# Kernel tuning notes

Measured on AMD Instinct MI355X. Metric: run time of the kernel, lower is better.

The kernel has to match this reference:

```python
import jax, jax.numpy as jnp
import numpy as np

B, S, C = 2, 2048, 512
E, H = 512, 8
HD = E // H
SCALE = HD ** -0.5


def setup_inputs() -> dict:
    key = jax.random.key(0)
    ks = jax.random.split(key, 10)
    s = 1.0 / np.sqrt(C)
    return {
        "x": jax.random.normal(ks[0], (B, S, C), dtype=jnp.float32),
        "dist_map": jax.random.uniform(ks[1], (B, H, S, S), dtype=jnp.float32),
        "mask": jax.random.randint(ks[2], (B, S), 0, 2, dtype=jnp.int32),
        "Wq": jax.random.normal(ks[3], (E, C), dtype=jnp.float32) * s,
        "bq": jnp.zeros((E,), dtype=jnp.float32),
        "Wk": jax.random.normal(ks[4], (E, C), dtype=jnp.float32) * s,
        "bk": jnp.zeros((E,), dtype=jnp.float32),
        "Wv": jax.random.normal(ks[5], (E, C), dtype=jnp.float32) * s,
        "bv": jnp.zeros((E,), dtype=jnp.float32),
        "Wo": jax.random.normal(ks[6], (E, E), dtype=jnp.float32) * (1.0 / np.sqrt(E)),
        "bo": jnp.zeros((E,), dtype=jnp.float32),
    }


def reference(x, dist_map, mask, Wq, bq, Wk, bk, Wv, bv, Wo, bo):
    # NOTE: faithful to original torch code: .view(B, H, S, HD) without transpose
    q = (x @ Wq.T + bq).reshape(B, H, S, HD)
    k = (x @ Wk.T + bk).reshape(B, H, S, HD)
    v = (x @ Wv.T + bv).reshape(B, H, S, HD)
    attn = jnp.einsum('bhqd,bhkd->bhqk', q, k)
    pad = mask.astype(bool)[:, None, None, :]  # [B,1,1,S]
    attn = jnp.where(pad, jnp.float32(-10000.0), attn)
    attn = jax.nn.softmax(attn * SCALE, axis=-1)
    attn = (attn + dist_map) * 0.5  # post-softmax dist_map blend
    # dropout p=0.0 -> identity
    attn_probs = attn
    ctx = jnp.einsum('bhal,bhlv->bhav', attn_probs, v)  # [B,H,S,HD]
    ctx = ctx.transpose(0, 2, 1, 3).reshape(B, S, E)
    out = ctx @ Wo.T + bo
    return (out, attn_probs)
```

## Files before the change

### kernel.cpp

```cpp
#include <hip/hip_runtime.h>
#include <stdint.h>

typedef __attribute__((ext_vector_type(4))) float  f32x4;
typedef __attribute__((ext_vector_type(8))) short  short8;
typedef __attribute__((ext_vector_type(4))) short  short4v;

#define MFMA16(a,b,c) __builtin_amdgcn_mfma_f32_16x16x32_bf16((a),(b),(c),0,0,0)

static __device__ __forceinline__ unsigned short f2bf(float f) {
    unsigned int u = __float_as_uint(f);
    u += 0x7FFFu + ((u >> 16) & 1u);
    return (unsigned short)(u >> 16);
}
static __device__ __forceinline__ float bflo(unsigned int v) { return __uint_as_float(v << 16); }
static __device__ __forceinline__ float bfhi(unsigned int v) { return __uint_as_float(v & 0xFFFF0000u); }
static __device__ __forceinline__ float bf2f(unsigned short v) { return __uint_as_float(((unsigned int)v) << 16); }
static __device__ __forceinline__ unsigned int packbf(float a, float b) {
    return (unsigned int)f2bf(a) | ((unsigned int)f2bf(b) << 16);
}


__global__ __launch_bounds__(256) void qkv_gemm(
    const float* __restrict__ x,
    const float* __restrict__ Wq, const float* __restrict__ bq,
    const float* __restrict__ Wk, const float* __restrict__ bk,
    const float* __restrict__ Wv, const float* __restrict__ bv,
    unsigned short* __restrict__ Qb, unsigned short* __restrict__ Kb,
    unsigned short* __restrict__ Vb)
{
    __shared__ unsigned short As[128 * 40];
    __shared__ unsigned short Bs[128 * 40];

    const int tid  = threadIdx.x;
    const int lane = tid & 63;
    const int wid  = tid >> 6;
    const int g = lane >> 4, c = lane & 15;
    const int wr = wid >> 1, wc = wid & 1;
    const int bm    = blockIdx.x;
    const int widx  = blockIdx.y >> 2;
    const int ntile = blockIdx.y & 3;

    const float* W    = (widx == 0) ? Wq : (widx == 1) ? Wk : Wv;
    const float* bias = (widx == 0) ? bq : (widx == 1) ? bk : bv;
    unsigned short* Y = (widx == 0) ? Qb : (widx == 1) ? Kb : Vb;
    const float* Abase = x + (size_t)bm * 128 * 512;
    const float* Bbase = W + (size_t)ntile * 128 * 512;

    f32x4 acc[4][4];
    #pragma unroll
    for (int m = 0; m < 4; m++)
        #pragma unroll
        for (int n = 0; n < 4; n++) acc[m][n] = (f32x4){0.f, 0.f, 0.f, 0.f};

    for (int kk = 0; kk < 512; kk += 32) {
        #pragma unroll
        for (int i = 0; i < 4; i++) {
            int f  = i * 256 + tid;
            int rr = f >> 3;
            int cc = (f & 7) * 4;
            f32x4 va = *(const f32x4*)(Abase + rr * 512 + kk + cc);
            f32x4 vb = *(const f32x4*)(Bbase + rr * 512 + kk + cc);
            short4v sa, sb;
            #pragma unroll
            for (int q = 0; q < 4; q++) { sa[q] = (short)f2bf(va[q]); sb[q] = (short)f2bf(vb[q]); }
            *(short4v*)(&As[rr * 40 + cc]) = sa;
            *(short4v*)(&Bs[rr * 40 + cc]) = sb;
        }
        __syncthreads();

        short8 af[4], bfr[4];
        #pragma unroll
        for (int m = 0; m < 4; m++) af[m]  = *(const short8*)(&As[(wr * 64 + m * 16 + c) * 40 + g * 8]);
        #pragma unroll
        for (int n = 0; n < 4; n++) bfr[n] = *(const short8*)(&Bs[(wc * 64 + n * 16 + c) * 40 + g * 8]);
        #pragma unroll
        for (int m = 0; m < 4; m++)
            #pragma unroll
            for (int n = 0; n < 4; n++)
                acc[m][n] = MFMA16(af[m], bfr[n], acc[m][n]);
        __syncthreads();
    }

    #pragma unroll
    for (int n = 0; n < 4; n++) {
        int colW = ntile * 128 + wc * 64 + n * 16 + c;
        float bb = bias[colW];
        #pragma unroll
        for (int m = 0; m < 4; m++) {
            #pragma unroll
            for (int r = 0; r < 4; r++) {
                int row = bm * 128 + wr * 64 + m * 16 + g * 4 + r;
                Y[(size_t)row * 512 + colW] = f2bf(acc[m][n][r] + bb);
            }
        }
    }
}

__global__ __launch_bounds__(256) void v_transpose(
    const unsigned short* __restrict__ Vb, unsigned short* __restrict__ Vt)
{
    __shared__ unsigned short T[8][520];

    const int tid = threadIdx.x;
    const int t   = blockIdx.x;
    const int bh  = blockIdx.y;
    const int b = bh >> 3, h = bh & 7;

    #pragma unroll
    for (int i = 0; i < 2; i++) {
        int idx = i * 256 + tid;
        int j   = idx >> 6;
        int cc  = (idx & 63) * 8;
        short8 v = *(const short8*)(Vb + (size_t)(b * 2048 + h * 256 + t * 8 + j) * 512 + cc);
        *(short8*)(&T[j][cc]) = v;
    }
    __syncthreads();

    const int d   = tid >> 2;
    const int sjb = (tid & 3) * 16;
    unsigned short tmp[16];
    #pragma unroll
    for (int i = 0; i < 16; i++) {
        int sj = sjb + i;
        tmp[i] = T[sj >> 3][(sj & 7) * 64 + d];
    }
    unsigned short* dst = Vt + ((size_t)(bh * 64 + d) * 2048) + t * 64 + sjb;
    *(short8*)(dst)     = *(short8*)(&tmp[0]);
    *(short8*)(dst + 8) = *(short8*)(&tmp[8]);
}

__global__ __launch_bounds__(256) void attn_kernel(
    const unsigned short* __restrict__ Qb, const unsigned short* __restrict__ Kb,
    const unsigned short* __restrict__ Vt,
    const float* __restrict__ dist, const int* __restrict__ mask,
    float* __restrict__ attn_out, unsigned short* __restrict__ ctx_bf)
{
    __shared__ float red[4][16];
    __shared__ __attribute__((aligned(16))) unsigned char SMEM[17408];
    unsigned short (*AP)[16][72] = (unsigned short (*)[16][72])SMEM;
    float (*Cred)[16][68] = (float (*)[16][68])SMEM;

    const int tid = threadIdx.x;
    const int lane = tid & 63, wid = tid >> 6;
    const int g = lane >> 4, c = lane & 15;

    const int wg  = blockIdx.x + gridDim.x * blockIdx.y;
    const int qg  = (wg >> 3) & 127;
    const int bh  = (wg & 7) * 2 + ((wg >> 10) & 1);
    const int b = bh >> 3, h = bh & 7;

    const unsigned short* Qh  = Qb + (size_t)b * 1048576 + (size_t)h * 131072;
    const unsigned short* Kh  = Kb + (size_t)b * 1048576 + (size_t)h * 131072;
    const unsigned short* Vth = Vt + (size_t)bh * 131072;
    const float* distb = dist + (size_t)bh * 4194304;
    float*       outb  = attn_out + (size_t)bh * 4194304;
    const int*   maskb = mask + b * 2048;

    const int qrow    = qg * 16;
    const int keybase = wid * 512;

    const float SC = 0.18033688011f;

    short8 qf[2];
    #pragma unroll
    for (int ks = 0; ks < 2; ks++)
        qf[ks] = *(const short8*)(Qh + (size_t)(qrow + c) * 64 + ks * 32 + g * 8);

    unsigned int pl[8][4][2];
    float dsum[4] = {0.f, 0.f, 0.f, 0.f};

    #pragma unroll
    for (int t = 0; t < 8; t++) {
        const int kb = keybase + t * 64;
        #pragma unroll
        for (int n = 0; n < 4; n++) {
            short8 k0 = *(const short8*)(Kh + (size_t)(kb + n * 16 + c) * 64 + g * 8);
            short8 k1 = *(const short8*)(Kh + (size_t)(kb + n * 16 + c) * 64 + 32 + g * 8);
            f32x4 z = (f32x4){0.f, 0.f, 0.f, 0.f};
            z = MFMA16(qf[0], k0, z);
            z = MFMA16(qf[1], k1, z);
            const int mv = maskb[kb + n * 16 + c];
            float e[4];
            #pragma unroll
            for (int r = 0; r < 4; r++) {
                float ex = exp2f(z[r] * SC);
                e[r] = mv ? 0.f : ex;
                dsum[r] += e[r];
            }
            pl[t][n][0] = packbf(e[0], e[1]);
            pl[t][n][1] = packbf(e[2], e[3]);
        }
    }
    #pragma unroll
    for (int r = 0; r < 4; r++) {
        #pragma unroll
        for (int off = 1; off < 16; off <<= 1)
            dsum[r] += __shfl_xor(dsum[r], off);
    }
    if (c == 0) {
        #pragma unroll
        for (int r = 0; r < 4; r++) red[wid][g * 4 + r] = dsum[r];
    }
    __syncthreads();
    float invd2[4];
    #pragma unroll
    for (int r = 0; r < 4; r++) {
        const int row = g * 4 + r;
        invd2[r] = 0.5f / (red[0][row] + red[1][row] + red[2][row] + red[3][row]);
    }

    f32x4 cacc[4];
    #pragma unroll
    for (int nd = 0; nd < 4; nd++) cacc[nd] = (f32x4){0.f, 0.f, 0.f, 0.f};

    #pragma unroll
    for (int t = 0; t < 8; t++) {
        const int kb = keybase + t * 64;

        f32x4 dv[4];
        #pragma unroll
        for (int rg = 0; rg < 4; rg++)
            dv[rg] = *(const f32x4*)(distb + (size_t)(qrow + rg * 4 + g) * 2048 + kb + c * 4);

        #pragma unroll
        for (int n = 0; n < 4; n++) {
            #pragma unroll
            for (int pi = 0; pi < 2; pi++) {
                unsigned int v = pl[t][n][pi];
                AP[wid][g * 4 + pi * 2    ][n * 16 + c] = f2bf(bflo(v) * invd2[pi * 2]);
                AP[wid][g * 4 + pi * 2 + 1][n * 16 + c] = f2bf(bfhi(v) * invd2[pi * 2 + 1]);
            }
        }

        #pragma unroll
        for (int rg = 0; rg < 4; rg++) {
            const int row = rg * 4 + g;
            short4v pv = *(const short4v*)(&AP[wid][row][c * 4]);
            f32x4 apv;
            #pragma unroll
            for (int q = 0; q < 4; q++)
                apv[q] = fmaf(dv[rg][q], 0.5f, bf2f((unsigned short)pv[q]));
            *(f32x4*)(outb + (size_t)(qrow + row) * 2048 + kb + c * 4) = apv;
            short4v apb;
            #pragma unroll
            for (int q = 0; q < 4; q++) apb[q] = (short)f2bf(apv[q]);
            *(short4v*)(&AP[wid][row][c * 4]) = apb;
        }

        short8 apf[2];
        #pragma unroll
        for (int ks = 0; ks < 2; ks++)
            apf[ks] = *(const short8*)(&AP[wid][c][ks * 32 + g * 8]);
        #pragma unroll
        for (int nd = 0; nd < 4; nd++) {
            #pragma unroll
            for (int ks = 0; ks < 2; ks++) {
                short8 vf = *(const short8*)(Vth + (size_t)(nd * 16 + c) * 2048 + kb + ks * 32 + g * 8);
                cacc[nd] = MFMA16(apf[ks], vf, cacc[nd]);
            }
        }
    }

    __syncthreads();
    #pragma unroll
    for (int nd = 0; nd < 4; nd++)
        #pragma unroll
        for (int r = 0; r < 4; r++)
            Cred[wid][g * 4 + r][nd * 16 + c] = cacc[nd][r];
    __syncthreads();

    {
        const int q  = tid >> 4;
        const int dq = (tid & 15) * 4;
        f32x4 s = *(const f32x4*)(&Cred[0][q][dq]);
        #pragma unroll
        for (int w = 1; w < 4; w++) {
            f32x4 t2 = *(const f32x4*)(&Cred[w][q][dq]);
            #pragma unroll
            for (int j = 0; j < 4; j++) s[j] += t2[j];
        }
        short4v cb;
        #pragma unroll
        for (int j = 0; j < 4; j++) cb[j] = (short)f2bf(s[j]);
        *(short4v*)(ctx_bf + (size_t)(b * 2048 + qrow + q) * 512 + h * 64 + dq) = cb;
    }
}

__global__ __launch_bounds__(256) void out_gemm(
    const unsigned short* __restrict__ A,
    const float* __restrict__ Wo, const float* __restrict__ bo,
    float* __restrict__ out)
{
    __shared__ unsigned short As[128 * 40];
    __shared__ unsigned short Bs[128 * 40];

    const int tid  = threadIdx.x;
    const int lane = tid & 63;
    const int wid  = tid >> 6;
    const int g = lane >> 4, c = lane & 15;
    const int wr = wid >> 1, wc = wid & 1;
    const int bm    = blockIdx.x;
    const int ntile = blockIdx.y;

    const unsigned short* Abase = A + (size_t)bm * 128 * 512;
    const float* Bbase = Wo + (size_t)ntile * 128 * 512;

    f32x4 acc[4][4];
    #pragma unroll
    for (int m = 0; m < 4; m++)
        #pragma unroll
        for (int n = 0; n < 4; n++) acc[m][n] = (f32x4){0.f, 0.f, 0.f, 0.f};

    for (int kk = 0; kk < 512; kk += 32) {
        #pragma unroll
        for (int i = 0; i < 2; i++) {
            int f8 = i * 256 + tid;
            int rr = f8 >> 2;
            int cc = (f8 & 3) * 8;
            short8 va = *(const short8*)(Abase + (size_t)rr * 512 + kk + cc);
            *(short8*)(&As[rr * 40 + cc]) = va;
        }
        #pragma unroll
        for (int i = 0; i < 4; i++) {
            int f  = i * 256 + tid;
            int rr = f >> 3;
            int cc = (f & 7) * 4;
            f32x4 vb = *(const f32x4*)(Bbase + (size_t)rr * 512 + kk + cc);
            short4v sb;
            #pragma unroll
            for (int q = 0; q < 4; q++) sb[q] = (short)f2bf(vb[q]);
            *(short4v*)(&Bs[rr * 40 + cc]) = sb;
        }
        __syncthreads();

        short8 af[4], bfr[4];
        #pragma unroll
        for (int m = 0; m < 4; m++) af[m]  = *(const short8*)(&As[(wr * 64 + m * 16 + c) * 40 + g * 8]);
        #pragma unroll
        for (int n = 0; n < 4; n++) bfr[n] = *(const short8*)(&Bs[(wc * 64 + n * 16 + c) * 40 + g * 8]);
        #pragma unroll
        for (int m = 0; m < 4; m++)
            #pragma unroll
            for (int n = 0; n < 4; n++)
                acc[m][n] = MFMA16(af[m], bfr[n], acc[m][n]);
        __syncthreads();
    }

    #pragma unroll
    for (int n = 0; n < 4; n++) {
        int col = ntile * 128 + wc * 64 + n * 16 + c;
        float bb = bo[col];
        #pragma unroll
        for (int m = 0; m < 4; m++) {
            #pragma unroll
            for (int r = 0; r < 4; r++) {
                int row = bm * 128 + wr * 64 + m * 16 + g * 4 + r;
                out[(size_t)row * 512 + col] = acc[m][n][r] + bb;
            }
        }
    }
}

extern "C" void kernel_launch(void* const* d_in, const int* in_sizes, int n_in,
                              void* d_out, int out_size, void* d_ws, size_t ws_size,
                              hipStream_t stream)
{
    const float* x    = (const float*)d_in[0];
    const float* dist = (const float*)d_in[1];
    const int*   mask = (const int*)d_in[2];
    const float* Wq   = (const float*)d_in[3];
    const float* bq   = (const float*)d_in[4];
    const float* Wk   = (const float*)d_in[5];
    const float* bk   = (const float*)d_in[6];
    const float* Wv   = (const float*)d_in[7];
    const float* bv   = (const float*)d_in[8];
    const float* Wo   = (const float*)d_in[9];
    const float* bo   = (const float*)d_in[10];

    float* out      = (float*)d_out;
    float* attn_out = out + 2097152;

    char* ws = (char*)d_ws;
    unsigned short* Qb  = (unsigned short*)(ws);
    unsigned short* Kb  = (unsigned short*)(ws + (4u << 20));
    unsigned short* Vb  = (unsigned short*)(ws + (8u << 20));
    unsigned short* Vt  = (unsigned short*)(ws + (12u << 20));
    unsigned short* ctx = (unsigned short*)(ws + (8u << 20));

    qkv_gemm   <<<dim3(32, 12), 256, 0, stream>>>(x, Wq, bq, Wk, bk, Wv, bv, Qb, Kb, Vb);
    v_transpose<<<dim3(32, 16), 256, 0, stream>>>(Vb, Vt);
    attn_kernel<<<dim3(128, 16), 256, 0, stream>>>(Qb, Kb, Vt, dist, mask, attn_out, ctx);
    out_gemm   <<<dim3(32, 4),  256, 0, stream>>>(ctx, Wo, bo, out);
}
```

Measured before the change: 256.2 us.

## Split attention into score/exp kernel and streaming PV kernel via workspace

Splits the fused attention kernel in two. The first kernel computes QK^T, applies the mask and exp, and writes the unnormalised bf16 probabilities plus the inverse row sums to a 128 MB workspace. The second kernel streams those probabilities back with dist_map, normalises them, writes attn_probs, and does the PV MFMA. The aim is to cut register pressure so each kernel runs at higher occupancy and streams memory better. The cost is an extra 128 MB write and read of intermediate data, plus a fallback path when the workspace is too small.

```diff
diff --git a/kernel.cpp b/kernel.cpp
--- a/kernel.cpp
+++ b/kernel.cpp
@@ -129,6 +129,190 @@
     *(short8*)(dst + 8) = *(short8*)(&tmp[8]);
 }
 
+__global__ __launch_bounds__(256) void attn_core(
+    const unsigned short* __restrict__ Qb, const unsigned short* __restrict__ Kb,
+    const int* __restrict__ mask,
+    unsigned int* __restrict__ Pws, float* __restrict__ Dws)
+{
+    __shared__ float red[4][16];
+
+    const int tid = threadIdx.x;
+    const int lane = tid & 63, wid = tid >> 6;
+    const int g = lane >> 4, c = lane & 15;
+
+    const int wg  = blockIdx.x + gridDim.x * blockIdx.y;
+    const int qg  = (wg >> 3) & 127;
+    const int bh  = (wg & 7) * 2 + ((wg >> 10) & 1);
+    const int b = bh >> 3, h = bh & 7;
+
+    const unsigned short* Qh = Qb + (size_t)b * 1048576 + (size_t)h * 131072;
+    const unsigned short* Kh = Kb + (size_t)b * 1048576 + (size_t)h * 131072;
+    const int* maskb = mask + b * 2048;
+
+    const int qrow    = qg * 16;
+    const int keybase = wid * 512;
+    const float SC = 0.18033688011f;
+
+    short8 qf[2];
+    #pragma unroll
+    for (int ks = 0; ks < 2; ks++)
+        qf[ks] = *(const short8*)(Qh + (size_t)(qrow + c) * 64 + ks * 32 + g * 8);
+
+    unsigned int* Pw = Pws + ((((size_t)bh * 128 + qg) * 4 + wid) * 8) * 512 + lane;
+
+    float dsum[4] = {0.f, 0.f, 0.f, 0.f};
+
+    #pragma unroll
+    for (int t = 0; t < 8; t++) {
+        const int kb = keybase + t * 64;
+        #pragma unroll
+        for (int n = 0; n < 4; n++) {
+            short8 k0 = *(const short8*)(Kh + (size_t)(kb + n * 16 + c) * 64 + g * 8);
+            short8 k1 = *(const short8*)(Kh + (size_t)(kb + n * 16 + c) * 64 + 32 + g * 8);
+            f32x4 z = (f32x4){0.f, 0.f, 0.f, 0.f};
+            z = MFMA16(qf[0], k0, z);
+            z = MFMA16(qf[1], k1, z);
+            const int mv = maskb[kb + n * 16 + c];
+            float e[4];
+            #pragma unroll
+            for (int r = 0; r < 4; r++) {
+                float ex = exp2f(z[r] * SC);
+                e[r] = mv ? 0.f : ex;
+                dsum[r] += e[r];
+            }
+            Pw[(size_t)t * 512 + (n * 2 + 0) * 64] = packbf(e[0], e[1]);
+            Pw[(size_t)t * 512 + (n * 2 + 1) * 64] = packbf(e[2], e[3]);
+        }
+    }
+    #pragma unroll
+    for (int r = 0; r < 4; r++) {
+        #pragma unroll
+        for (int off = 1; off < 16; off <<= 1)
+            dsum[r] += __shfl_xor(dsum[r], off);
+    }
+    if (c == 0) {
+        #pragma unroll
+        for (int r = 0; r < 4; r++) red[wid][g * 4 + r] = dsum[r];
+    }
+    __syncthreads();
+    if (tid < 16) {
+        float D = red[0][tid] + red[1][tid] + red[2][tid] + red[3][tid];
+        Dws[(size_t)bh * 2048 + qrow + tid] = 0.5f / D;
+    }
+}
+
+__global__ __launch_bounds__(256) void stream_pv(
+    const unsigned int* __restrict__ Pws, const float* __restrict__ Dws,
+    const unsigned short* __restrict__ Vt, const float* __restrict__ dist,
+    float* __restrict__ attn_out, unsigned short* __restrict__ ctx_bf)
+{
+    __shared__ __attribute__((aligned(16))) unsigned char SMEM[17408];
+    unsigned short (*AP)[16][72] = (unsigned short (*)[16][72])SMEM;
+    float (*Cred)[16][68] = (float (*)[16][68])SMEM;
+
+    const int tid = threadIdx.x;
+    const int lane = tid & 63, wid = tid >> 6;
+    const int g = lane >> 4, c = lane & 15;
+
+    const int wg  = blockIdx.x + gridDim.x * blockIdx.y;
+    const int qg  = (wg >> 3) & 127;
+    const int bh  = (wg & 7) * 2 + ((wg >> 10) & 1);
+    const int b = bh >> 3, h = bh & 7;
+
+    const unsigned short* Vth = Vt + (size_t)bh * 131072;
+    const float* distb = dist + (size_t)bh * 4194304;
+    float*       outb  = attn_out + (size_t)bh * 4194304;
+
+    const int qrow    = qg * 16;
+    const int keybase = wid * 512;
+
+    float invd2[4];
+    #pragma unroll
+    for (int r = 0; r < 4; r++)
+        invd2[r] = Dws[(size_t)bh * 2048 + qrow + g * 4 + r];
+
+    const unsigned int* Pr = Pws + ((((size_t)bh * 128 + qg) * 4 + wid) * 8) * 512 + lane;
+
+    f32x4 cacc[4];
+    #pragma unroll
+    for (int nd = 0; nd < 4; nd++) cacc[nd] = (f32x4){0.f, 0.f, 0.f, 0.f};
+
+    #pragma unroll
+    for (int t = 0; t < 8; t++) {
+        const int kb = keybase + t * 64;
+
+        unsigned int plv[8];
+        #pragma unroll
+        for (int j = 0; j < 8; j++) plv[j] = Pr[(size_t)t * 512 + j * 64];
+        f32x4 dv[4];
+        #pragma unroll
+        for (int rg = 0; rg < 4; rg++)
+            dv[rg] = *(const f32x4*)(distb + (size_t)(qrow + rg * 4 + g) * 2048 + kb + c * 4);
+
+        #pragma unroll
+        for (int n = 0; n < 4; n++) {
+            #pragma unroll
+            for (int pi = 0; pi < 2; pi++) {
+                unsigned int v = plv[n * 2 + pi];
+                AP[wid][g * 4 + pi * 2    ][n * 16 + c] = f2bf(bflo(v) * invd2[pi * 2]);
+                AP[wid][g * 4 + pi * 2 + 1][n * 16 + c] = f2bf(bfhi(v) * invd2[pi * 2 + 1]);
+            }
+        }
+
+        #pragma unroll
+        for (int rg = 0; rg < 4; rg++) {
+            const int row = rg * 4 + g;
+            short4v pv = *(const short4v*)(&AP[wid][row][c * 4]);
+            f32x4 apv;
+            #pragma unroll
+            for (int q = 0; q < 4; q++)
+                apv[q] = fmaf(dv[rg][q], 0.5f, bf2f((unsigned short)pv[q]));
+            *(f32x4*)(outb + (size_t)(qrow + row) * 2048 + kb + c * 4) = apv;
+            short4v apb;
+            #pragma unroll
+            for (int q = 0; q < 4; q++) apb[q] = (short)f2bf(apv[q]);
+            *(short4v*)(&AP[wid][row][c * 4]) = apb;
+        }
+
+        short8 apf[2];
+        #pragma unroll
+        for (int ks = 0; ks < 2; ks++)
+            apf[ks] = *(const short8*)(&AP[wid][c][ks * 32 + g * 8]);
+        #pragma unroll
+        for (int nd = 0; nd < 4; nd++) {
+            #pragma unroll
+            for (int ks = 0; ks < 2; ks++) {
+                short8 vf = *(const short8*)(Vth + (size_t)(nd * 16 + c) * 2048 + kb + ks * 32 + g * 8);
+                cacc[nd] = MFMA16(apf[ks], vf, cacc[nd]);
+            }
+        }
+    }
+
+    __syncthreads();
+    #pragma unroll
+    for (int nd = 0; nd < 4; nd++)
+        #pragma unroll
+        for (int r = 0; r < 4; r++)
+            Cred[wid][g * 4 + r][nd * 16 + c] = cacc[nd][r];
+    __syncthreads();
+
+    {
+        const int q  = tid >> 4;
+        const int dq = (tid & 15) * 4;
+        f32x4 s = *(const f32x4*)(&Cred[0][q][dq]);
+        #pragma unroll
+        for (int w = 1; w < 4; w++) {
+            f32x4 t2 = *(const f32x4*)(&Cred[w][q][dq]);
+            #pragma unroll
+            for (int j = 0; j < 4; j++) s[j] += t2[j];
+        }
+        short4v cb;
+        #pragma unroll
+        for (int j = 0; j < 4; j++) cb[j] = (short)f2bf(s[j]);
+        *(short4v*)(ctx_bf + (size_t)(b * 2048 + qrow + q) * 512 + h * 64 + dq) = cb;
+    }
+}
+
 __global__ __launch_bounds__(256) void attn_kernel(
     const unsigned short* __restrict__ Qb, const unsigned short* __restrict__ Kb,
     const unsigned short* __restrict__ Vt,
@@ -158,7 +342,6 @@
 
     const int qrow    = qg * 16;
     const int keybase = wid * 512;
-
     const float SC = 0.18033688011f;
 
     short8 qf[2];
@@ -387,8 +570,22 @@
     unsigned short* Vt  = (unsigned short*)(ws + (12u << 20));
     unsigned short* ctx = (unsigned short*)(ws + (8u << 20));
 
+    const size_t PW_OFF   = (size_t)16 << 20;
+    const size_t PW_BYTES = (size_t)134217728;
+    const size_t DW_OFF   = PW_OFF + PW_BYTES;
+    const size_t NEED     = DW_OFF + (size_t)131072;
+
     qkv_gemm   <<<dim3(32, 12), 256, 0, stream>>>(x, Wq, bq, Wk, bk, Wv, bv, Qb, Kb, Vb);
     v_transpose<<<dim3(32, 16), 256, 0, stream>>>(Vb, Vt);
-    attn_kernel<<<dim3(128, 16), 256, 0, stream>>>(Qb, Kb, Vt, dist, mask, attn_out, ctx);
+
+    if (ws_size >= NEED) {
+        unsigned int* Pws = (unsigned int*)(ws + PW_OFF);
+        float*        Dws = (float*)(ws + DW_OFF);
+        attn_core <<<dim3(128, 16), 256, 0, stream>>>(Qb, Kb, mask, Pws, Dws);
+        stream_pv <<<dim3(128, 16), 256, 0, stream>>>(Pws, Dws, Vt, dist, attn_out, ctx);
+    } else {
+        attn_kernel<<<dim3(128, 16), 256, 0, stream>>>(Qb, Kb, Vt, dist, mask, attn_out, ctx);
+    }
+
     out_gemm   <<<dim3(32, 4),  256, 0, stream>>>(ctx, Wo, bo, out);
 }
```

New measurement: 312.4 us. 1.22x slower.
